# Kernel tuning notes

Measured on AMD Instinct MI355X. Metric: run time of the kernel, lower is better.

The kernel has to match this reference:

```python
import jax, jax.numpy as jnp
import numpy as np

B, C, H, W = 16, 64, 64, 64
N_CODES = 4096


def setup_inputs() -> dict:
    key = jax.random.key(0)
    k1, k2 = jax.random.split(key)
    z = jax.random.normal(k1, (B, C, H, W), dtype=jnp.float32)
    emb = jax.random.normal(k2, (N_CODES, C), dtype=jnp.float32)
    return {"z": z, "emb": emb}


def reference(z, emb):
    b, c, h, w = z.shape
    embf = emb.astype(jnp.float32)
    # (b, c, h, w) -> (N, c) flattened tokens
    zf = jnp.transpose(z, (0, 2, 3, 1)).reshape(-1, c).astype(jnp.float32)
    # squared L2 distances: ||z||^2 - 2 z.e + ||e||^2, shape (N, n_codes)
    d = (
        jnp.sum(zf * zf, axis=1, keepdims=True)
        - 2.0 * (zf @ embf.T)
        + jnp.sum(embf * embf, axis=1)
    )
    idx = jnp.argmin(d, axis=1)  # (N,)
    zq = embf[idx].reshape(b, h, w, c)
    zq = jnp.transpose(zq, (0, 3, 1, 2))
    return zq.astype(z.dtype)
```

## Files before the change

### kernel.cpp

```cpp
#include <hip/hip_runtime.h>


typedef __attribute__((ext_vector_type(8))) short short8;
typedef __attribute__((ext_vector_type(4))) float f32x4;
typedef unsigned int u32;

#define NCHUNK 256
#define FRAGS 6
#define CHUNK_WSB (FRAGS * 64 * 16)
#define WSB_BYTES (NCHUNK * CHUNK_WSB)
#define OFF_N    WSB_BYTES
#define OFF_CNT  (OFF_N + 16384)
#define OFF_LIST (OFF_CNT + 64)
#define WS_NEEDED ((size_t)OFF_LIST + 65536u * 4u)
#define DELTA 0.005f

static __device__ __forceinline__ unsigned short f2bf(float f) {
    u32 u = __builtin_bit_cast(u32, f);
    u += 0x7fffu + ((u >> 16) & 1u);
    return (unsigned short)(u >> 16);
}
static __device__ __forceinline__ float bf2f(unsigned short h) {
    u32 u = ((u32)h) << 16;
    return __builtin_bit_cast(float, u);
}

__global__ void vq_pack_kernel(const float* __restrict__ emb,
                               unsigned short* __restrict__ wsB,
                               float* __restrict__ wsN,
                               u32* __restrict__ wsCnt) {
    int ck    = blockIdx.x;
    int f     = threadIdx.x >> 6;
    int lane  = threadIdx.x & 63;
    int level = f >> 1, s = f & 1;
    int code  = ck * 16 + (lane & 15);
    int kb    = s * 32 + (lane >> 4) * 8;
    const float* src = emb + code * 64 + kb;
    short8 o;
#pragma unroll
    for (int j = 0; j < 8; ++j) {
        float x = src[j];
        unsigned short h1 = f2bf(x);
        float r1 = x - bf2f(h1);
        unsigned short h2 = f2bf(r1);
        float r2 = r1 - bf2f(h2);
        unsigned short h3 = f2bf(r2);
        o[j] = (short)(level == 0 ? h1 : (level == 1 ? h2 : h3));
    }
    ((short8*)wsB)[(ck * FRAGS + f) * 64 + lane] = o;

    if (threadIdx.x < 16) {
        int c = ck * 16 + threadIdx.x;
        const float* e = emb + c * 64;
        float ssum = 0.f;
#pragma unroll
        for (int k = 0; k < 64; ++k) { float v = e[k]; ssum = fmaf(v, v, ssum); }
        wsN[c] = -0.5f * ssum;
    }
    if (ck == 0 && threadIdx.x == 0) *wsCnt = 0u;
}

__global__ __launch_bounds__(256, 2) void vq_main_kernel(
    const float* __restrict__ z, const float* __restrict__ emb,
    const unsigned short* __restrict__ wsB, const float* __restrict__ wsN,
    u32* __restrict__ wsCnt, u32* __restrict__ wsList,
    float* __restrict__ out)
{
    __shared__ float sS1[2][128], sS2[2][128];
    __shared__ int   sI1[2][128];
    __shared__ int   sOut[128];

    const int wave = threadIdx.x >> 6;
    const int lane = threadIdx.x & 63;
    const int quad = lane >> 4;
    const int col  = lane & 15;
    const int tg   = wave >> 1;
    const int half = wave & 1;
    const int cbase = half * 128;

    const int t0 = blockIdx.x * 128 + tg * 64;
    short8 a[4][2][2];
#pragma unroll
    for (int t = 0; t < 4; ++t) {
        const int tok = t0 + t * 16 + col;
        const int b   = tok >> 12;
        const int hw  = tok & 4095;
        const float* zp = z + b * 262144 + hw;
#pragma unroll
        for (int s = 0; s < 2; ++s)
#pragma unroll
            for (int j = 0; j < 8; ++j) {
                int k = s * 32 + quad * 8 + j;
                float x = zp[k * 4096];
                unsigned short h1 = f2bf(x);
                a[t][0][s][j] = (short)h1;
                a[t][1][s][j] = (short)f2bf(x - bf2f(h1));
            }
    }

    float best[4][4], best2[4][4];
    int   bidx[4][4];
#pragma unroll
    for (int t = 0; t < 4; ++t)
#pragma unroll
        for (int r = 0; r < 4; ++r) {
            best[t][r] = -3.4e38f; best2[t][r] = -3.4e38f; bidx[t][r] = 0;
        }

    const short8* Bg = (const short8*)wsB;
    auto loadB = [&](short8* B, int i) {
        const short8* p = Bg + (size_t)(cbase + i) * (FRAGS * 64) + lane;
        B[0] = p[0 * 64];
        B[1] = p[1 * 64];
        B[2] = p[2 * 64];
        B[3] = p[3 * 64];
    };
    auto ldn = [&](int i) { return wsN[(cbase + i) * 16 + col]; };

    auto compute = [&](const short8* B, float nrm, int i) {
        const int code = (cbase + i) * 16 + col;
#pragma unroll
        for (int t = 0; t < 4; ++t) {
            f32x4 acc = {nrm, nrm, nrm, nrm};
            acc = __builtin_amdgcn_mfma_f32_16x16x32_bf16(a[t][1][0], B[0], acc, 0, 0, 0);
            acc = __builtin_amdgcn_mfma_f32_16x16x32_bf16(a[t][1][1], B[1], acc, 0, 0, 0);
            acc = __builtin_amdgcn_mfma_f32_16x16x32_bf16(a[t][0][0], B[2], acc, 0, 0, 0);
            acc = __builtin_amdgcn_mfma_f32_16x16x32_bf16(a[t][0][1], B[3], acc, 0, 0, 0);
            acc = __builtin_amdgcn_mfma_f32_16x16x32_bf16(a[t][0][0], B[0], acc, 0, 0, 0);
            acc = __builtin_amdgcn_mfma_f32_16x16x32_bf16(a[t][0][1], B[1], acc, 0, 0, 0);
#pragma unroll
            for (int r = 0; r < 4; ++r) {
                float sc = acc[r];
                best2[t][r] = fmaxf(best2[t][r], fminf(sc, best[t][r]));
                bool gt = sc > best[t][r];
                bidx[t][r] = gt ? code : bidx[t][r];
                best[t][r] = fmaxf(best[t][r], sc);
            }
        }
    };

    short8 B0[4], B1[4];
    float  n0, n1;
    loadB(B0, 0); n0 = ldn(0);
    for (int i = 0; i < 128; i += 2) {
        loadB(B1, i + 1); n1 = ldn(i + 1);
        compute(B0, n0, i);
        if (i + 2 < 128) { loadB(B0, i + 2); n0 = ldn(i + 2); }
        compute(B1, n1, i + 1);
    }

#pragma unroll
    for (int off = 1; off < 16; off <<= 1)
#pragma unroll
        for (int t = 0; t < 4; ++t)
#pragma unroll
            for (int r = 0; r < 4; ++r) {
                float os1 = __shfl_xor(best[t][r],  off, 64);
                int   oi1 = __shfl_xor(bidx[t][r],  off, 64);
                float os2 = __shfl_xor(best2[t][r], off, 64);
                bool take = (os1 > best[t][r]) ||
                            (os1 == best[t][r] && oi1 < bidx[t][r]);
                float ns2 = take ? fmaxf(best[t][r], os2)
                                 : fmaxf(best2[t][r], os1);
                if (take) { best[t][r] = os1; bidx[t][r] = oi1; }
                best2[t][r] = ns2;
            }
    if (col == 0)
#pragma unroll
        for (int t = 0; t < 4; ++t)
#pragma unroll
            for (int r = 0; r < 4; ++r) {
                int tokb = tg * 64 + t * 16 + quad * 4 + r;
                sS1[half][tokb] = best[t][r];
                sS2[half][tokb] = best2[t][r];
                sI1[half][tokb] = bidx[t][r];
            }
    __syncthreads();

    if (threadIdx.x < 128) {
        const int tk = threadIdx.x;
        float b0 = sS1[0][tk], b1 = sS1[1][tk];
        int   i0 = sI1[0][tk], i1 = sI1[1][tk];
        float q0 = sS2[0][tk], q1 = sS2[1][tk];
        bool take1 = b1 > b0;
        float bw = take1 ? b1 : b0;
        float bl = take1 ? b0 : b1;
        float qw = take1 ? q1 : q0;
        sOut[tk] = take1 ? i1 : i0;
        float second = fmaxf(qw, bl);
        if (bw - second < DELTA) {
            u32 slot = atomicAdd(wsCnt, 1u);
            wsList[slot] = (u32)(blockIdx.x * 128 + tk);
        }
    }
    __syncthreads();

    const int tk   = threadIdx.x & 127;
    const int coff = (threadIdx.x >> 7) * 32;
    const int gt   = blockIdx.x * 128 + tk;
    const int ob   = gt >> 12, ohw = gt & 4095;
    float* op = out + ob * 262144 + ohw;
    const float4* ep = (const float4*)(emb + sOut[tk] * 64 + coff);
#pragma unroll
    for (int i = 0; i < 8; ++i) {
        float4 v = ep[i];
        op[(coff + 4 * i + 0) * 4096] = v.x;
        op[(coff + 4 * i + 1) * 4096] = v.y;
        op[(coff + 4 * i + 2) * 4096] = v.z;
        op[(coff + 4 * i + 3) * 4096] = v.w;
    }
}

__global__ __launch_bounds__(256) void vq_fix_kernel(
    const float* __restrict__ z, const float* __restrict__ emb,
    const unsigned short* __restrict__ wsB, const float* __restrict__ wsN,
    const u32* __restrict__ wsCnt, const u32* __restrict__ wsList,
    float* __restrict__ out)
{
    __shared__ float sS[4][16];
    __shared__ int   sI[4][16];
    __shared__ int   sTok[16];

    const int wave = threadIdx.x >> 6;
    const int lane = threadIdx.x & 63;
    const int quad = lane >> 4;
    const int col  = lane & 15;
    const u32 count = *wsCnt;
    const u32 tiles = (count + 15u) >> 4;

    for (u32 T = blockIdx.x; T < tiles; T += gridDim.x) {
        if (threadIdx.x < 16) {
            u32 slot = T * 16 + threadIdx.x;
            if (slot >= count) slot = count - 1;
            sTok[threadIdx.x] = (int)wsList[slot];
        }
        __syncthreads();

        const int tok = sTok[col];
        const int b   = tok >> 12;
        const int hw  = tok & 4095;
        const float* zp = z + b * 262144 + hw;
        short8 a[3][2];
#pragma unroll
        for (int s = 0; s < 2; ++s)
#pragma unroll
            for (int j = 0; j < 8; ++j) {
                int k = s * 32 + quad * 8 + j;
                float x = zp[k * 4096];
                unsigned short h1 = f2bf(x);
                float r1 = x - bf2f(h1);
                unsigned short h2 = f2bf(r1);
                float r2 = r1 - bf2f(h2);
                a[0][s][j] = (short)h1;
                a[1][s][j] = (short)h2;
                a[2][s][j] = (short)f2bf(r2);
            }

        float best[4] = {-3.4e38f, -3.4e38f, -3.4e38f, -3.4e38f};
        int   bidx[4] = {0, 0, 0, 0};

        const short8* Bg = (const short8*)wsB;
        for (int ck = wave * 64; ck < wave * 64 + 64; ++ck) {
            const size_t fb = (size_t)ck * (FRAGS * 64);
            short8 b10 = Bg[fb + 0 * 64 + lane];
            short8 b11 = Bg[fb + 1 * 64 + lane];
            short8 b20 = Bg[fb + 2 * 64 + lane];
            short8 b21 = Bg[fb + 3 * 64 + lane];
            short8 b30 = Bg[fb + 4 * 64 + lane];
            short8 b31 = Bg[fb + 5 * 64 + lane];
            const float nnrm = wsN[ck * 16 + col];
            const int   code = ck * 16 + col;

            f32x4 accA = {0.f, 0.f, 0.f, 0.f};
            f32x4 accB = {0.f, 0.f, 0.f, 0.f};
            accA = __builtin_amdgcn_mfma_f32_16x16x32_bf16(a[1][0], b20, accA, 0, 0, 0);
            accB = __builtin_amdgcn_mfma_f32_16x16x32_bf16(a[0][0], b20, accB, 0, 0, 0);
            accA = __builtin_amdgcn_mfma_f32_16x16x32_bf16(a[1][1], b21, accA, 0, 0, 0);
            accB = __builtin_amdgcn_mfma_f32_16x16x32_bf16(a[0][1], b21, accB, 0, 0, 0);
            accA = __builtin_amdgcn_mfma_f32_16x16x32_bf16(a[0][0], b30, accA, 0, 0, 0);
            accB = __builtin_amdgcn_mfma_f32_16x16x32_bf16(a[1][0], b10, accB, 0, 0, 0);
            accA = __builtin_amdgcn_mfma_f32_16x16x32_bf16(a[0][1], b31, accA, 0, 0, 0);
            accB = __builtin_amdgcn_mfma_f32_16x16x32_bf16(a[1][1], b11, accB, 0, 0, 0);
            accA = __builtin_amdgcn_mfma_f32_16x16x32_bf16(a[2][0], b10, accA, 0, 0, 0);
            accB = __builtin_amdgcn_mfma_f32_16x16x32_bf16(a[0][0], b10, accB, 0, 0, 0);
            accA = __builtin_amdgcn_mfma_f32_16x16x32_bf16(a[2][1], b11, accA, 0, 0, 0);
            accB = __builtin_amdgcn_mfma_f32_16x16x32_bf16(a[0][1], b11, accB, 0, 0, 0);

#pragma unroll
            for (int r = 0; r < 4; ++r) {
                float score = (accA[r] + accB[r]) + nnrm;
                if (score > best[r]) { best[r] = score; bidx[r] = code; }
            }
        }

#pragma unroll
        for (int off = 1; off < 16; off <<= 1)
#pragma unroll
            for (int r = 0; r < 4; ++r) {
                float os = __shfl_xor(best[r], off, 64);
                int   oi = __shfl_xor(bidx[r], off, 64);
                if (os > best[r] || (os == best[r] && oi < bidx[r])) {
                    best[r] = os; bidx[r] = oi;
                }
            }
        if (col == 0)
#pragma unroll
            for (int r = 0; r < 4; ++r) {
                sS[wave][quad * 4 + r] = best[r];
                sI[wave][quad * 4 + r] = bidx[r];
            }
        __syncthreads();

        if (threadIdx.x < 16) {
            float bs = sS[0][threadIdx.x]; int bi = sI[0][threadIdx.x];
#pragma unroll
            for (int w = 1; w < 4; ++w) {
                float s2 = sS[w][threadIdx.x]; int i2 = sI[w][threadIdx.x];
                if (s2 > bs || (s2 == bs && i2 < bi)) { bs = s2; bi = i2; }
            }
            sI[0][threadIdx.x] = bi;
        }
        __syncthreads();

        {
            const int row = threadIdx.x & 15;
            const int cb  = (threadIdx.x >> 4) * 4;
            const int tk2 = sTok[row];
            const int bb  = tk2 >> 12, hh = tk2 & 4095;
            const float* e = emb + sI[0][row] * 64;
            float* op = out + bb * 262144 + hh;
#pragma unroll
            for (int i = 0; i < 4; ++i)
                op[(cb + i) * 4096] = e[cb + i];
        }
        __syncthreads();
    }
}

__global__ __launch_bounds__(256) void vq_fp32_kernel(
    const float* __restrict__ z, const float* __restrict__ emb,
    float* __restrict__ out)
{
    __shared__ float se[64 * 64];
    __shared__ float snorm[64];

    const int t  = blockIdx.x * 256 + threadIdx.x;
    const int b  = t >> 12;
    const int hw = t & 4095;
    const float* zt = z + (size_t)b * 262144 + hw;
    float zf[64];
#pragma unroll
    for (int c = 0; c < 64; ++c) zf[c] = zt[(size_t)c * 4096];

    float best = -3.4e38f;
    int   bestIdx = 0;
    for (int k0 = 0; k0 < 4096; k0 += 64) {
        __syncthreads();
        const float4* src = (const float4*)(emb + (size_t)k0 * 64);
        float4*       dst = (float4*)se;
#pragma unroll
        for (int i = 0; i < 4; ++i)
            dst[i * 256 + threadIdx.x] = src[i * 256 + threadIdx.x];
        __syncthreads();
        if (threadIdx.x < 64) {
            float s = 0.f;
#pragma unroll
            for (int c = 0; c < 64; ++c) {
                float v = se[threadIdx.x * 64 + c];
                s = fmaf(v, v, s);
            }
            snorm[threadIdx.x] = 0.5f * s;
        }
        __syncthreads();
#pragma unroll 4
        for (int kk = 0; kk < 64; ++kk) {
            float dot = 0.f;
#pragma unroll
            for (int c = 0; c < 64; ++c)
                dot = fmaf(zf[c], se[kk * 64 + c], dot);
            float score = dot - snorm[kk];
            if (score > best) { best = score; bestIdx = k0 + kk; }
        }
    }
    const float* e  = emb + (size_t)bestIdx * 64;
    float*       ot = out + (size_t)b * 262144 + hw;
#pragma unroll
    for (int c = 0; c < 64; ++c) ot[(size_t)c * 4096] = e[c];
}

extern "C" void kernel_launch(void* const* d_in, const int* in_sizes, int n_in,
                              void* d_out, int out_size, void* d_ws, size_t ws_size,
                              hipStream_t stream) {
    const float* z   = (const float*)d_in[0];
    const float* emb = (const float*)d_in[1];
    float*       out = (float*)d_out;

    if (ws_size < WS_NEEDED) {
        vq_fp32_kernel<<<256, 256, 0, stream>>>(z, emb, out);
        return;
    }

    unsigned short* wsB   = (unsigned short*)d_ws;
    float*          wsN   = (float*)((char*)d_ws + OFF_N);
    u32*            wsCnt = (u32*)((char*)d_ws + OFF_CNT);
    u32*            wsList= (u32*)((char*)d_ws + OFF_LIST);

    vq_pack_kernel<<<256, 384, 0, stream>>>(emb, wsB, wsN, wsCnt);
    vq_main_kernel<<<512, 256, 0, stream>>>(z, emb, wsB, wsN, wsCnt, wsList, out);
    vq_fix_kernel<<<256, 256, 0, stream>>>(z, emb, wsB, wsN, wsCnt, wsList, out);
}
```

Baseline: 212.3 us.

## Fuse ambiguous-token refinement into main kernel with per-block shared list

The separate fix kernel and global atomic worklist are removed. Each main-kernel block now collects its near-tie tokens in a shared-memory list and rescans the full codebook for them with higher-precision split-bf16 MFMAs, using double-buffered fragment loads, before finishing. This drops one kernel launch, the global atomic counter and the workspace list. The cost is that blocks holding many ambiguous tokens run longer and create tail imbalance, and the shared-memory use adds pressure. The second-best tracking also moves to a single fmed3 instruction.

```diff
diff --git a/kernel.cpp b/kernel.cpp
--- a/kernel.cpp
+++ b/kernel.cpp
@@ -10,9 +10,7 @@
 #define CHUNK_WSB (FRAGS * 64 * 16)
 #define WSB_BYTES (NCHUNK * CHUNK_WSB)
 #define OFF_N    WSB_BYTES
-#define OFF_CNT  (OFF_N + 16384)
-#define OFF_LIST (OFF_CNT + 64)
-#define WS_NEEDED ((size_t)OFF_LIST + 65536u * 4u)
+#define WS_NEEDED ((size_t)OFF_N + 16384u)
 #define DELTA 0.005f
 
 static __device__ __forceinline__ unsigned short f2bf(float f) {
@@ -27,8 +25,7 @@
 
 __global__ void vq_pack_kernel(const float* __restrict__ emb,
                                unsigned short* __restrict__ wsB,
-                               float* __restrict__ wsN,
-                               u32* __restrict__ wsCnt) {
+                               float* __restrict__ wsN) {
     int ck    = blockIdx.x;
     int f     = threadIdx.x >> 6;
     int lane  = threadIdx.x & 63;
@@ -57,18 +54,20 @@
         for (int k = 0; k < 64; ++k) { float v = e[k]; ssum = fmaf(v, v, ssum); }
         wsN[c] = -0.5f * ssum;
     }
-    if (ck == 0 && threadIdx.x == 0) *wsCnt = 0u;
 }
 
 __global__ __launch_bounds__(256, 2) void vq_main_kernel(
     const float* __restrict__ z, const float* __restrict__ emb,
     const unsigned short* __restrict__ wsB, const float* __restrict__ wsN,
-    u32* __restrict__ wsCnt, u32* __restrict__ wsList,
     float* __restrict__ out)
 {
     __shared__ float sS1[2][128], sS2[2][128];
     __shared__ int   sI1[2][128];
     __shared__ int   sOut[128];
+    __shared__ int   sUList[128];
+    __shared__ int   sUCnt;
+    __shared__ float sRS[4][16];
+    __shared__ int   sRI[4][16];
 
     const int wave = threadIdx.x >> 6;
     const int lane = threadIdx.x & 63;
@@ -77,6 +76,8 @@
     const int tg   = wave >> 1;
     const int half = wave & 1;
     const int cbase = half * 128;
+
+    if (threadIdx.x == 0) sUCnt = 0;
 
     const int t0 = blockIdx.x * 128 + tg * 64;
     short8 a[4][2][2];
@@ -131,7 +132,7 @@
 #pragma unroll
             for (int r = 0; r < 4; ++r) {
                 float sc = acc[r];
-                best2[t][r] = fmaxf(best2[t][r], fminf(sc, best[t][r]));
+                best2[t][r] = __builtin_amdgcn_fmed3f(sc, best[t][r], best2[t][r]);
                 bool gt = sc > best[t][r];
                 bidx[t][r] = gt ? code : bidx[t][r];
                 best[t][r] = fmaxf(best[t][r], sc);
@@ -189,145 +190,135 @@
         sOut[tk] = take1 ? i1 : i0;
         float second = fmaxf(qw, bl);
         if (bw - second < DELTA) {
-            u32 slot = atomicAdd(wsCnt, 1u);
-            wsList[slot] = (u32)(blockIdx.x * 128 + tk);
+            int s = atomicAdd(&sUCnt, 1);
+            sUList[s] = tk;
         }
     }
     __syncthreads();
 
-    const int tk   = threadIdx.x & 127;
-    const int coff = (threadIdx.x >> 7) * 32;
-    const int gt   = blockIdx.x * 128 + tk;
-    const int ob   = gt >> 12, ohw = gt & 4095;
-    float* op = out + ob * 262144 + ohw;
-    const float4* ep = (const float4*)(emb + sOut[tk] * 64 + coff);
-#pragma unroll
-    for (int i = 0; i < 8; ++i) {
-        float4 v = ep[i];
-        op[(coff + 4 * i + 0) * 4096] = v.x;
-        op[(coff + 4 * i + 1) * 4096] = v.y;
-        op[(coff + 4 * i + 2) * 4096] = v.z;
-        op[(coff + 4 * i + 3) * 4096] = v.w;
-    }
-}
-
-__global__ __launch_bounds__(256) void vq_fix_kernel(
-    const float* __restrict__ z, const float* __restrict__ emb,
-    const unsigned short* __restrict__ wsB, const float* __restrict__ wsN,
-    const u32* __restrict__ wsCnt, const u32* __restrict__ wsList,
-    float* __restrict__ out)
-{
-    __shared__ float sS[4][16];
-    __shared__ int   sI[4][16];
-    __shared__ int   sTok[16];
-
-    const int wave = threadIdx.x >> 6;
-    const int lane = threadIdx.x & 63;
-    const int quad = lane >> 4;
-    const int col  = lane & 15;
-    const u32 count = *wsCnt;
-    const u32 tiles = (count + 15u) >> 4;
-
-    for (u32 T = blockIdx.x; T < tiles; T += gridDim.x) {
-        if (threadIdx.x < 16) {
-            u32 slot = T * 16 + threadIdx.x;
-            if (slot >= count) slot = count - 1;
-            sTok[threadIdx.x] = (int)wsList[slot];
-        }
-        __syncthreads();
-
-        const int tok = sTok[col];
-        const int b   = tok >> 12;
-        const int hw  = tok & 4095;
-        const float* zp = z + b * 262144 + hw;
-        short8 a[3][2];
+    {
+        const int tk   = threadIdx.x & 127;
+        const int coff = (threadIdx.x >> 7) * 32;
+        const int gt   = blockIdx.x * 128 + tk;
+        const int ob   = gt >> 12, ohw = gt & 4095;
+        float* op = out + ob * 262144 + ohw;
+        const float4* ep = (const float4*)(emb + sOut[tk] * 64 + coff);
+#pragma unroll
+        for (int i = 0; i < 8; ++i) {
+            float4 v = ep[i];
+            op[(coff + 4 * i + 0) * 4096] = v.x;
+            op[(coff + 4 * i + 1) * 4096] = v.y;
+            op[(coff + 4 * i + 2) * 4096] = v.z;
+            op[(coff + 4 * i + 3) * 4096] = v.w;
+        }
+    }
+    __syncthreads();
+
+    const int cnt = sUCnt;
+    for (int T0 = 0; T0 < cnt; T0 += 16) {
+        int slot = T0 + col;
+        if (slot >= cnt) slot = cnt - 1;
+        const int tokb = sUList[slot];
+        const int gt2  = blockIdx.x * 128 + tokb;
+        const int b2   = gt2 >> 12, hw2 = gt2 & 4095;
+        const float* zp2 = z + b2 * 262144 + hw2;
+
+        short8 af[3][2];
 #pragma unroll
         for (int s = 0; s < 2; ++s)
 #pragma unroll
             for (int j = 0; j < 8; ++j) {
                 int k = s * 32 + quad * 8 + j;
-                float x = zp[k * 4096];
+                float x = zp2[k * 4096];
                 unsigned short h1 = f2bf(x);
                 float r1 = x - bf2f(h1);
                 unsigned short h2 = f2bf(r1);
                 float r2 = r1 - bf2f(h2);
-                a[0][s][j] = (short)h1;
-                a[1][s][j] = (short)h2;
-                a[2][s][j] = (short)f2bf(r2);
-            }
-
-        float best[4] = {-3.4e38f, -3.4e38f, -3.4e38f, -3.4e38f};
-        int   bidx[4] = {0, 0, 0, 0};
-
-        const short8* Bg = (const short8*)wsB;
-        for (int ck = wave * 64; ck < wave * 64 + 64; ++ck) {
-            const size_t fb = (size_t)ck * (FRAGS * 64);
-            short8 b10 = Bg[fb + 0 * 64 + lane];
-            short8 b11 = Bg[fb + 1 * 64 + lane];
-            short8 b20 = Bg[fb + 2 * 64 + lane];
-            short8 b21 = Bg[fb + 3 * 64 + lane];
-            short8 b30 = Bg[fb + 4 * 64 + lane];
-            short8 b31 = Bg[fb + 5 * 64 + lane];
+                af[0][s][j] = (short)h1;
+                af[1][s][j] = (short)h2;
+                af[2][s][j] = (short)f2bf(r2);
+            }
+
+        float rb[4] = {-3.4e38f, -3.4e38f, -3.4e38f, -3.4e38f};
+        int   ri[4] = {0, 0, 0, 0};
+
+        auto ldf = [&](short8* F, int ck) {
+            const short8* p = Bg + (size_t)ck * (FRAGS * 64) + lane;
+#pragma unroll
+            for (int q = 0; q < 6; ++q) F[q] = p[q * 64];
+        };
+        auto rstep = [&](const short8* F, int ck) {
             const float nnrm = wsN[ck * 16 + col];
             const int   code = ck * 16 + col;
-
             f32x4 accA = {0.f, 0.f, 0.f, 0.f};
             f32x4 accB = {0.f, 0.f, 0.f, 0.f};
-            accA = __builtin_amdgcn_mfma_f32_16x16x32_bf16(a[1][0], b20, accA, 0, 0, 0);
-            accB = __builtin_amdgcn_mfma_f32_16x16x32_bf16(a[0][0], b20, accB, 0, 0, 0);
-            accA = __builtin_amdgcn_mfma_f32_16x16x32_bf16(a[1][1], b21, accA, 0, 0, 0);
-            accB = __builtin_amdgcn_mfma_f32_16x16x32_bf16(a[0][1], b21, accB, 0, 0, 0);
-            accA = __builtin_amdgcn_mfma_f32_16x16x32_bf16(a[0][0], b30, accA, 0, 0, 0);
-            accB = __builtin_amdgcn_mfma_f32_16x16x32_bf16(a[1][0], b10, accB, 0, 0, 0);
-            accA = __builtin_amdgcn_mfma_f32_16x16x32_bf16(a[0][1], b31, accA, 0, 0, 0);
-            accB = __builtin_amdgcn_mfma_f32_16x16x32_bf16(a[1][1], b11, accB, 0, 0, 0);
-            accA = __builtin_amdgcn_mfma_f32_16x16x32_bf16(a[2][0], b10, accA, 0, 0, 0);
-            accB = __builtin_amdgcn_mfma_f32_16x16x32_bf16(a[0][0], b10, accB, 0, 0, 0);
-            accA = __builtin_amdgcn_mfma_f32_16x16x32_bf16(a[2][1], b11, accA, 0, 0, 0);
-            accB = __builtin_amdgcn_mfma_f32_16x16x32_bf16(a[0][1], b11, accB, 0, 0, 0);
-
+            accA = __builtin_amdgcn_mfma_f32_16x16x32_bf16(af[1][0], F[2], accA, 0, 0, 0);
+            accB = __builtin_amdgcn_mfma_f32_16x16x32_bf16(af[0][0], F[2], accB, 0, 0, 0);
+            accA = __builtin_amdgcn_mfma_f32_16x16x32_bf16(af[1][1], F[3], accA, 0, 0, 0);
+            accB = __builtin_amdgcn_mfma_f32_16x16x32_bf16(af[0][1], F[3], accB, 0, 0, 0);
+            accA = __builtin_amdgcn_mfma_f32_16x16x32_bf16(af[0][0], F[4], accA, 0, 0, 0);
+            accB = __builtin_amdgcn_mfma_f32_16x16x32_bf16(af[1][0], F[0], accB, 0, 0, 0);
+            accA = __builtin_amdgcn_mfma_f32_16x16x32_bf16(af[0][1], F[5], accA, 0, 0, 0);
+            accB = __builtin_amdgcn_mfma_f32_16x16x32_bf16(af[1][1], F[1], accB, 0, 0, 0);
+            accA = __builtin_amdgcn_mfma_f32_16x16x32_bf16(af[2][0], F[0], accA, 0, 0, 0);
+            accB = __builtin_amdgcn_mfma_f32_16x16x32_bf16(af[0][0], F[0], accB, 0, 0, 0);
+            accA = __builtin_amdgcn_mfma_f32_16x16x32_bf16(af[2][1], F[1], accA, 0, 0, 0);
+            accB = __builtin_amdgcn_mfma_f32_16x16x32_bf16(af[0][1], F[1], accB, 0, 0, 0);
 #pragma unroll
             for (int r = 0; r < 4; ++r) {
                 float score = (accA[r] + accB[r]) + nnrm;
-                if (score > best[r]) { best[r] = score; bidx[r] = code; }
-            }
+                if (score > rb[r]) { rb[r] = score; ri[r] = code; }
+            }
+        };
+
+        const int ck0 = wave * 64;
+        short8 F0[6], F1[6];
+        ldf(F0, ck0);
+        for (int i = 0; i < 64; i += 2) {
+            ldf(F1, ck0 + i + 1);
+            rstep(F0, ck0 + i);
+            if (i + 2 < 64) ldf(F0, ck0 + i + 2);
+            rstep(F1, ck0 + i + 1);
         }
 
 #pragma unroll
         for (int off = 1; off < 16; off <<= 1)
 #pragma unroll
             for (int r = 0; r < 4; ++r) {
-                float os = __shfl_xor(best[r], off, 64);
-                int   oi = __shfl_xor(bidx[r], off, 64);
-                if (os > best[r] || (os == best[r] && oi < bidx[r])) {
-                    best[r] = os; bidx[r] = oi;
+                float os = __shfl_xor(rb[r], off, 64);
+                int   oi = __shfl_xor(ri[r], off, 64);
+                if (os > rb[r] || (os == rb[r] && oi < ri[r])) {
+                    rb[r] = os; ri[r] = oi;
                 }
             }
         if (col == 0)
 #pragma unroll
             for (int r = 0; r < 4; ++r) {
-                sS[wave][quad * 4 + r] = best[r];
-                sI[wave][quad * 4 + r] = bidx[r];
+                sRS[wave][quad * 4 + r] = rb[r];
+                sRI[wave][quad * 4 + r] = ri[r];
             }
         __syncthreads();
 
         if (threadIdx.x < 16) {
-            float bs = sS[0][threadIdx.x]; int bi = sI[0][threadIdx.x];
+            float bs = sRS[0][threadIdx.x]; int bi = sRI[0][threadIdx.x];
 #pragma unroll
             for (int w = 1; w < 4; ++w) {
-                float s2 = sS[w][threadIdx.x]; int i2 = sI[w][threadIdx.x];
+                float s2 = sRS[w][threadIdx.x]; int i2 = sRI[w][threadIdx.x];
                 if (s2 > bs || (s2 == bs && i2 < bi)) { bs = s2; bi = i2; }
             }
-            sI[0][threadIdx.x] = bi;
+            sRI[0][threadIdx.x] = bi;
         }
         __syncthreads();
 
         {
             const int row = threadIdx.x & 15;
+            int rslot = T0 + row;
+            if (rslot >= cnt) rslot = cnt - 1;
             const int cb  = (threadIdx.x >> 4) * 4;
-            const int tk2 = sTok[row];
-            const int bb  = tk2 >> 12, hh = tk2 & 4095;
-            const float* e = emb + sI[0][row] * 64;
+            const int tk2 = sUList[rslot];
+            const int g3  = blockIdx.x * 128 + tk2;
+            const int bb  = g3 >> 12, hh = g3 & 4095;
+            const float* e = emb + sRI[0][row] * 64;
             float* op = out + bb * 262144 + hh;
 #pragma unroll
             for (int i = 0; i < 4; ++i)
@@ -400,12 +391,9 @@
         return;
     }
 
-    unsigned short* wsB   = (unsigned short*)d_ws;
-    float*          wsN   = (float*)((char*)d_ws + OFF_N);
-    u32*            wsCnt = (u32*)((char*)d_ws + OFF_CNT);
-    u32*            wsList= (u32*)((char*)d_ws + OFF_LIST);
-
-    vq_pack_kernel<<<256, 384, 0, stream>>>(emb, wsB, wsN, wsCnt);
-    vq_main_kernel<<<512, 256, 0, stream>>>(z, emb, wsB, wsN, wsCnt, wsList, out);
-    vq_fix_kernel<<<256, 256, 0, stream>>>(z, emb, wsB, wsN, wsCnt, wsList, out);
-}
+    unsigned short* wsB = (unsigned short*)d_ws;
+    float*          wsN = (float*)((char*)d_ws + OFF_N);
+
+    vq_pack_kernel<<<256, 384, 0, stream>>>(emb, wsB, wsN);
+    vq_main_kernel<<<512, 256, 0, stream>>>(z, emb, wsB, wsN, out);
+}
```

New measurement: 189.9 us. 1.12x faster.
